# Performance work log

Hardware: AMD Instinct MI355X
Metric: run time of the kernel (lower is better)

The kernel has to match this reference:

```python
import jax, jax.numpy as jnp
import numpy as np

N = 20000
E = 320000
D_IN = 256
D = 128
H = 4
L = 2
NUM_CLASSES = 7
LN_EPS = 1e-5


def setup_inputs() -> dict:
    key = jax.random.key(0)
    ks = jax.random.split(key, 12)
    inp = {}
    inp["x"] = jax.random.normal(ks[0], (N, D_IN), dtype=jnp.float32)
    inp["edge_index"] = jax.random.randint(ks[1], (2, E), 0, N, dtype=jnp.int32)
    inp["W_in"] = jax.random.normal(ks[2], (D_IN, D), dtype=jnp.float32) / np.sqrt(D_IN)
    inp["b_in"] = jnp.zeros((D,), jnp.float32)
    inp["Wq"] = jax.random.normal(ks[3], (L, D, H * D), dtype=jnp.float32) / np.sqrt(D)
    inp["bq"] = jnp.zeros((L, H * D), jnp.float32)
    inp["Wk"] = jax.random.normal(ks[4], (L, D, H * D), dtype=jnp.float32) / np.sqrt(D)
    inp["bk"] = jnp.zeros((L, H * D), jnp.float32)
    inp["Wv"] = jax.random.normal(ks[5], (L, D, H * D), dtype=jnp.float32) / np.sqrt(D)
    inp["bv"] = jnp.zeros((L, H * D), jnp.float32)
    inp["Wskip"] = jax.random.normal(ks[6], (L, D, D), dtype=jnp.float32) / np.sqrt(D)
    inp["bskip"] = jnp.zeros((L, D), jnp.float32)
    inp["ln_g"] = jnp.ones((L, D), jnp.float32)
    inp["ln_b"] = jnp.zeros((L, D), jnp.float32)
    inp["Wc"] = jax.random.normal(ks[7], (D, NUM_CLASSES), dtype=jnp.float32) / np.sqrt(D)
    inp["bc"] = jnp.zeros((NUM_CLASSES,), jnp.float32)
    return inp


def degree_pe(edge_index):
    # degree of source nodes (edge_index[0]), then sinusoidal encoding of the degree
    deg = jax.ops.segment_sum(jnp.ones((E,), jnp.float32), edge_index[0], num_segments=N)
    i = jnp.arange(D, dtype=jnp.float32)
    freq = deg[:, None] / jnp.power(10000.0, i / D)[None, :]  # [N, D]
    return jnp.where((jnp.arange(D) % 2 == 0)[None, :], jnp.sin(freq), jnp.cos(freq))


def transformer_conv(xf, edge_index, Wq, bq, Wk, bk, Wv, bv, Wskip, bskip):
    # PyG TransformerConv: heads=H, concat=False (mean over heads), root_weight=True
    src, dst = edge_index[0], edge_index[1]
    q = (xf @ Wq + bq).reshape(N, H, D)
    k = (xf @ Wk + bk).reshape(N, H, D)
    v = (xf @ Wv + bv).reshape(N, H, D)
    qe = q[dst]                        # [E, H, D]
    ke = k[src]
    ve = v[src]
    scores = jnp.sum(qe * ke, axis=-1) / np.sqrt(D)  # [E, H]
    m = jax.ops.segment_max(scores, dst, num_segments=N)        # [N, H]
    p = jnp.exp(scores - m[dst])
    s = jax.ops.segment_sum(p, dst, num_segments=N)              # [N, H]
    alpha = p / (s[dst] + 1e-16)
    agg = jax.ops.segment_sum(alpha[:, :, None] * ve, dst, num_segments=N)  # [N, H, D]
    out = jnp.mean(agg, axis=1)       # concat=False -> average heads
    return out + xf @ Wskip + bskip   # root skip connection


def layer_norm(x, g, b):
    mu = jnp.mean(x, axis=-1, keepdims=True)
    var = jnp.mean(jnp.square(x - mu), axis=-1, keepdims=True)
    return (x - mu) * jax.lax.rsqrt(var + LN_EPS) * g + b


def reference(x, edge_index, W_in, b_in, Wq, bq, Wk, bk, Wv, bv, Wskip, bskip, ln_g, ln_b, Wc, bc):
    h = x @ W_in + b_in
    h = h + degree_pe(edge_index)
    for l in range(L):
        h_new = transformer_conv(h, edge_index, Wq[l], bq[l], Wk[l], bk[l], Wv[l], bv[l], Wskip[l], bskip[l])
        h = layer_norm(h + h_new, ln_g[l], ln_b[l])
        if l < L - 1:
            h = jax.nn.relu(h)
    return h @ Wc + bc  # [N, num_classes]
```

## Files before the change

kernel.cpp:

```cpp
#include <hip/hip_runtime.h>
#include <math.h>

#define NN 20000
#define EE 320000
#define DIN 256
#define DD 128
#define HHEADS 4
#define NCLS 7

typedef __attribute__((ext_vector_type(8))) __bf16 bf16x8;
typedef __attribute__((ext_vector_type(4))) float f32x4;
typedef __attribute__((ext_vector_type(2))) float f32x2;

__device__ __forceinline__ unsigned short f2bf(float f) {
  union { float f; unsigned int u; } c; c.f = f;
  unsigned int r = c.u + 0x7fffu + ((c.u >> 16) & 1u);
  return (unsigned short)(r >> 16);
}
__device__ __forceinline__ __bf16 f2bf16(float f) {
  union { unsigned short u; __bf16 b; } cv; cv.u = f2bf(f); return cv.b;
}
__device__ __forceinline__ unsigned char fp8enc(float v) {
  return (unsigned char)(__builtin_amdgcn_cvt_pk_fp8_f32(v, 0.f, 0, false) & 0xff);
}

__global__ void zero_ints(int* __restrict__ p, int n) {
  int i = blockIdx.x * blockDim.x + threadIdx.x;
  if (i < n) p[i] = 0;
}

__global__ void count_kernel(const int* __restrict__ ei, int* __restrict__ deg_src,
                             int* __restrict__ cnt_dst) {
  int e = blockIdx.x * blockDim.x + threadIdx.x;
  if (e >= EE) return;
  atomicAdd(&deg_src[ei[e]], 1);
  atomicAdd(&cnt_dst[ei[EE + e]], 1);
}

__global__ __launch_bounds__(1024) void scan_kernel(const int* __restrict__ cnt,
                                                    int* __restrict__ row_ptr,
                                                    int* __restrict__ fillp) {
  __shared__ int wsum[16];
  __shared__ int carry_s;
  const int tid = threadIdx.x;
  const int wid = tid >> 6, lane = tid & 63;
  if (tid == 0) carry_s = 0;
  __syncthreads();
  for (int base = 0; base < NN; base += 1024) {
    int i = base + tid;
    int x = (i < NN) ? cnt[i] : 0;
    int v = x;
#pragma unroll
    for (int off = 1; off < 64; off <<= 1) {
      int t = __shfl_up(v, off);
      if (lane >= off) v += t;
    }
    if (lane == 63) wsum[wid] = v;
    __syncthreads();
    int woff = 0;
    for (int w = 0; w < wid; ++w) woff += wsum[w];
    int excl = carry_s + woff + v - x;
    if (i < NN) { row_ptr[i] = excl; fillp[i] = excl; }
    __syncthreads();
    if (tid == 1023) carry_s += woff + v;
    __syncthreads();
  }
  if (tid == 0) row_ptr[NN] = EE;
}

__global__ void scatter_kernel(const int* __restrict__ ei, int* __restrict__ fillp,
                               int* __restrict__ ssrc) {
  int e = blockIdx.x * blockDim.x + threadIdx.x;
  if (e >= EE) return;
  int s = ei[e], d = ei[EE + e];
  int pos = atomicAdd(&fillp[d], 1);
  ssrc[pos] = s;
}

__global__ void pack_weights(const float* __restrict__ W_in, const float* __restrict__ Wq,
                             const float* __restrict__ Wk, const float* __restrict__ Wv,
                             const float* __restrict__ Wsk, const float* __restrict__ Wc,
                             __bf16* __restrict__ WT) {
  int idx = blockIdx.x * blockDim.x + threadIdx.x;
  if (idx >= 460800) return;
  float val;
  if (idx < 32768) {
    int m = idx >> 8, k = idx & 255;
    val = W_in[k * 128 + m];
  } else if (idx < 458752) {
    int t = idx - 32768;
    int l = t / 212992; int t2 = t - l * 212992;
    int r = t2 >> 7, kk = t2 & 127;
    if (r < 512)       val = Wq[l * 65536 + kk * 512 + r];
    else if (r < 1024) val = Wk[l * 65536 + kk * 512 + (r - 512)];
    else if (r < 1536) val = Wv[l * 65536 + kk * 512 + (r - 1024)];
    else               val = Wsk[l * 16384 + kk * 128 + (r - 1536)];
  } else {
    int t = idx - 458752;
    int r = t >> 7, kk = t & 127;
    val = (r < NCLS) ? Wc[kk * NCLS + r] : 0.f;
  }
  WT[idx] = f2bf16(val);
}

__global__ void pack_bias(const float* __restrict__ bq, const float* __restrict__ bk,
                          const float* __restrict__ bv, const float* __restrict__ bsk,
                          const float* __restrict__ bc, float* __restrict__ bcomb,
                          float* __restrict__ bcpad) {
  int idx = blockIdx.x * blockDim.x + threadIdx.x;
  if (idx < 3328) {
    int l = idx / 1664, r = idx % 1664;
    float v;
    if (r < 512)       v = bq[l * 512 + r];
    else if (r < 1024) v = bk[l * 512 + (r - 512)];
    else if (r < 1536) v = bv[l * 512 + (r - 1024)];
    else               v = bsk[l * 128 + (r - 1536)];
    bcomb[idx] = v;
  } else if (idx < 3344) {
    int r = idx - 3328;
    bcpad[r] = (r < NCLS) ? bc[r] : 0.f;
  }
}

__global__ __launch_bounds__(256) void mfma_gemm_in(
    const float* __restrict__ A, const __bf16* __restrict__ BT,
    const float* __restrict__ bias, float* __restrict__ o_f32,
    __bf16* __restrict__ o_bf0, const int* __restrict__ deg) {
  constexpr int K = 256;
  __shared__ __attribute__((aligned(16))) __bf16 As[64][136];
  __shared__ __attribute__((aligned(16))) __bf16 Bs[128][136];
  const int tid = threadIdx.x;
  const int brow = blockIdx.x * 64;
  const int wave = tid >> 6, lane = tid & 63;
  const int wm = wave & 1, wn = wave >> 1;
  const int lm = lane & 15, lk = (lane >> 4) * 8;
  const int srow16 = tid >> 4;
  const int sc8 = (tid & 15) * 8;
  f32x4 acc[2][4] = {};
  for (int k0 = 0; k0 < K; k0 += 128) {
    if (k0) __syncthreads();
#pragma unroll
    for (int t = 0; t < 4; ++t) {
      int row = t * 16 + srow16;
      int arow = brow + row;
      arow = (arow < NN) ? arow : (NN - 1);
      const float* ap = A + (size_t)arow * K + k0 + sc8;
      float4 a0 = *(const float4*)ap, a1 = *(const float4*)(ap + 4);
      uint4 w;
      w.x = (unsigned)f2bf(a0.x) | ((unsigned)f2bf(a0.y) << 16);
      w.y = (unsigned)f2bf(a0.z) | ((unsigned)f2bf(a0.w) << 16);
      w.z = (unsigned)f2bf(a1.x) | ((unsigned)f2bf(a1.y) << 16);
      w.w = (unsigned)f2bf(a1.z) | ((unsigned)f2bf(a1.w) << 16);
      *reinterpret_cast<uint4*>(&As[row][sc8]) = w;
    }
#pragma unroll
    for (int t = 0; t < 8; ++t) {
      int row = t * 16 + srow16;
      *reinterpret_cast<uint4*>(&Bs[row][sc8]) =
          *reinterpret_cast<const uint4*>(BT + (size_t)row * K + k0 + sc8);
    }
    __syncthreads();
#pragma unroll
    for (int ks = 0; ks < 4; ++ks) {
      bf16x8 af[2], bfr[4];
#pragma unroll
      for (int i = 0; i < 2; ++i)
        af[i] = *reinterpret_cast<const bf16x8*>(&As[wm * 32 + i * 16 + lm][ks * 32 + lk]);
#pragma unroll
      for (int j = 0; j < 4; ++j)
        bfr[j] = *reinterpret_cast<const bf16x8*>(&Bs[wn * 64 + j * 16 + lm][ks * 32 + lk]);
#pragma unroll
      for (int i = 0; i < 2; ++i)
#pragma unroll
        for (int j = 0; j < 4; ++j)
          acc[i][j] = __builtin_amdgcn_mfma_f32_16x16x32_bf16(af[i], bfr[j], acc[i][j], 0, 0, 0);
    }
  }
#pragma unroll
  for (int i = 0; i < 2; ++i) {
#pragma unroll
    for (int j = 0; j < 4; ++j) {
      const int col = wn * 64 + j * 16 + lm;
      const float bb = bias[col];
#pragma unroll
      for (int r = 0; r < 4; ++r) {
        const int row = brow + wm * 32 + i * 16 + (lane >> 4) * 4 + r;
        if (row >= NN) continue;
        float val = acc[i][j][r] + bb;
        float dg = (float)deg[row];
        float freq = dg * __expf(-0.07195578415606394f * (float)col);
        val += (col & 1) ? __cosf(freq) : __sinf(freq);
        o_f32[(size_t)row * DD + col] = val;
        o_bf0[(size_t)row * DD + col] = f2bf16(val);
      }
    }
  }
}

__global__ __launch_bounds__(512) void mfma_gemm_qkv(
    const __bf16* __restrict__ A, const __bf16* __restrict__ BT,
    const float* __restrict__ bias, const float* __restrict__ resid,
    __bf16* __restrict__ o_q, unsigned char* __restrict__ o_fp8,
    float* __restrict__ o_hs) {
  __shared__ __attribute__((aligned(16))) __bf16 Bs[128][136];
  const int tid = threadIdx.x;
  const int brow = blockIdx.x * 128;
  const int bcol = blockIdx.y * 128;
  const int wave = tid >> 6, lane = tid & 63;
  const int wm = wave & 3, wn = wave >> 2;
  const int lm = lane & 15, lk = (lane >> 4) * 8, l4 = (lane >> 4) * 4;
  const int srow32 = tid >> 4;
  const int sc8 = (tid & 15) * 8;

  uint4 breg[4];
#pragma unroll
  for (int t = 0; t < 4; ++t)
    breg[t] = *reinterpret_cast<const uint4*>(BT + (size_t)(bcol + t * 32 + srow32) * 128 + sc8);

  bf16x8 af[2][4];
#pragma unroll
  for (int i = 0; i < 2; ++i) {
    int row = brow + wm * 32 + i * 16 + lm;
    row = (row < NN) ? row : (NN - 1);
    const __bf16* ap = A + (size_t)row * 128 + lk;
#pragma unroll
    for (int ks = 0; ks < 4; ++ks)
      af[i][ks] = *reinterpret_cast<const bf16x8*>(ap + ks * 32);
  }

#pragma unroll
  for (int t = 0; t < 4; ++t)
    *reinterpret_cast<uint4*>(&Bs[t * 32 + srow32][sc8]) = breg[t];
  __syncthreads();

  f32x4 acc[2][4] = {};
#pragma unroll
  for (int ks = 0; ks < 4; ++ks) {
    bf16x8 bfr[4];
#pragma unroll
    for (int j = 0; j < 4; ++j)
      bfr[j] = *reinterpret_cast<const bf16x8*>(&Bs[wn * 64 + j * 16 + lm][ks * 32 + lk]);
#pragma unroll
    for (int i = 0; i < 2; ++i)
#pragma unroll
      for (int j = 0; j < 4; ++j)
        acc[i][j] = __builtin_amdgcn_mfma_f32_16x16x32_bf16(af[i][ks], bfr[j], acc[i][j], 0, 0, 0);
  }

#pragma unroll
  for (int i = 0; i < 2; ++i) {
#pragma unroll
    for (int j = 0; j < 4; ++j) {
      const int col = bcol + wn * 64 + j * 16 + lm;
      const float bb = bias[col];
#pragma unroll
      for (int r = 0; r < 4; ++r) {
        const int row = brow + wm * 32 + i * 16 + l4 + r;
        if (row >= NN) continue;
        float val = acc[i][j][r] + bb;
        if (col < 512) {
          o_q[(size_t)row * 512 + col] = f2bf16(val);
        } else if (col < 1024) {
          int dim = col - 512;
          o_fp8[(size_t)row * 1024 + (dim >> 3) * 16 + (dim & 7)] = fp8enc(val);
        } else if (col < 1536) {
          int dim = col - 1024;
          o_fp8[(size_t)row * 1024 + (dim >> 3) * 16 + 8 + (dim & 7)] = fp8enc(val);
        } else {
          o_hs[(size_t)row * DD + (col - 1536)] =
              val + resid[(size_t)row * DD + (col - 1536)];
        }
      }
    }
  }
}

__global__ __launch_bounds__(256) void mfma_gemm_cls(
    const __bf16* __restrict__ A, const __bf16* __restrict__ BT,
    const float* __restrict__ bias, float* __restrict__ out) {
  __shared__ __attribute__((aligned(16))) __bf16 Bs[16][136];
  const int tid = threadIdx.x;
  const int wave = tid >> 6, lane = tid & 63;
  const int lm = lane & 15, lk = (lane >> 4) * 8, l4 = (lane >> 4) * 4;
  const int brow = blockIdx.x * 128 + wave * 32;
  {
    int srow = tid >> 4, sc8 = (tid & 15) * 8;
    *reinterpret_cast<uint4*>(&Bs[srow][sc8]) =
        *reinterpret_cast<const uint4*>(BT + (size_t)srow * 128 + sc8);
  }
  __syncthreads();
  bf16x8 af[2][4];
#pragma unroll
  for (int i = 0; i < 2; ++i) {
    int row = brow + i * 16 + lm;
    row = (row < NN) ? row : (NN - 1);
    const __bf16* ap = A + (size_t)row * 128 + lk;
#pragma unroll
    for (int ks = 0; ks < 4; ++ks) af[i][ks] = *reinterpret_cast<const bf16x8*>(ap + ks * 32);
  }
  f32x4 acc[2] = {};
#pragma unroll
  for (int ks = 0; ks < 4; ++ks) {
    bf16x8 bfr = *reinterpret_cast<const bf16x8*>(&Bs[lm][ks * 32 + lk]);
#pragma unroll
    for (int i = 0; i < 2; ++i)
      acc[i] = __builtin_amdgcn_mfma_f32_16x16x32_bf16(af[i][ks], bfr, acc[i], 0, 0, 0);
  }
  if (lm < NCLS) {
    const float bb = bias[lm];
#pragma unroll
    for (int i = 0; i < 2; ++i) {
#pragma unroll
      for (int r = 0; r < 4; ++r) {
        int row = brow + i * 16 + l4 + r;
        if (row < NN) out[(size_t)row * NCLS + lm] = acc[i][r] + bb;
      }
    }
  }
}

__device__ __forceinline__ uint4 loadkv(const unsigned char* __restrict__ kv,
                                        const int* __restrict__ ssrc, int ee, int lane) {
  return *reinterpret_cast<const uint4*>(kv + (size_t)ssrc[ee] * 1024 + lane * 16);
}
__device__ __forceinline__ float qdot8(const f32x2 (&qv)[4], unsigned kx, unsigned ky) {
  f32x2 kd0 = __builtin_amdgcn_cvt_pk_f32_fp8((int)kx, false);
  f32x2 kd1 = __builtin_amdgcn_cvt_pk_f32_fp8((int)kx, true);
  f32x2 kd2 = __builtin_amdgcn_cvt_pk_f32_fp8((int)ky, false);
  f32x2 kd3 = __builtin_amdgcn_cvt_pk_f32_fp8((int)ky, true);
  f32x2 d2 = qv[0] * kd0;
  d2 = qv[1] * kd1 + d2;
  d2 = qv[2] * kd2 + d2;
  d2 = qv[3] * kd3 + d2;
  float d = d2[0] + d2[1];
  d += __shfl_xor(d, 1);
  d += __shfl_xor(d, 2);
  d += __shfl_xor(d, 4);
  d += __shfl_xor(d, 8);
  return d;
}
__device__ __forceinline__ void accum8(f32x2 (&a)[4], float& m, float& s, float sc,
                                       unsigned vz, unsigned vw) {
  if (sc > m) {
    float c = __expf(m - sc);
    f32x2 c2 = {c, c};
    s *= c;
#pragma unroll
    for (int d = 0; d < 4; ++d) a[d] *= c2;
    m = sc;
  }
  float w = __expf(sc - m);
  s += w;
  f32x2 w2 = {w, w};
  f32x2 vd0 = __builtin_amdgcn_cvt_pk_f32_fp8((int)vz, false);
  f32x2 vd1 = __builtin_amdgcn_cvt_pk_f32_fp8((int)vz, true);
  f32x2 vd2 = __builtin_amdgcn_cvt_pk_f32_fp8((int)vw, false);
  f32x2 vd3 = __builtin_amdgcn_cvt_pk_f32_fp8((int)vw, true);
  a[0] = w2 * vd0 + a[0];
  a[1] = w2 * vd1 + a[1];
  a[2] = w2 * vd2 + a[2];
  a[3] = w2 * vd3 + a[3];
}

__global__ __launch_bounds__(256) void attn_fused(
    const __bf16* __restrict__ qb, const unsigned char* __restrict__ kv,
    const float* __restrict__ hs,
    const int* __restrict__ row_ptr, const int* __restrict__ ssrc,
    const float* __restrict__ ln_g, const float* __restrict__ ln_b,
    float* __restrict__ h_out, __bf16* __restrict__ hb_out, int relu_flag) {
  const int node = blockIdx.x * 4 + (threadIdx.x >> 6);
  const int lane = threadIdx.x & 63;
  const int grp = lane >> 4, l16 = lane & 15;
  const int e0 = row_ptr[node], e1 = row_ptr[node + 1];
  const float scale = 0.088388347648318447f;

  f32x2 qv[4];
  {
    uint4 qw = *reinterpret_cast<const uint4*>(qb + (size_t)node * 512 + lane * 8);
    union { unsigned u; float f; } c;
    c.u = qw.x << 16; qv[0][0] = c.f; c.u = qw.x & 0xffff0000u; qv[0][1] = c.f;
    c.u = qw.y << 16; qv[1][0] = c.f; c.u = qw.y & 0xffff0000u; qv[1][1] = c.f;
    c.u = qw.z << 16; qv[2][0] = c.f; c.u = qw.z & 0xffff0000u; qv[2][1] = c.f;
    c.u = qw.w << 16; qv[3][0] = c.f; c.u = qw.w & 0xffff0000u; qv[3][1] = c.f;
  }
  float m = -INFINITY, s = 0.f;
  f32x2 a[4] = {};

  uint4 w0, w1, w2, w3;
  if (e0 + 0 < e1) w0 = loadkv(kv, ssrc, e0 + 0, lane);
  if (e0 + 1 < e1) w1 = loadkv(kv, ssrc, e0 + 1, lane);
  if (e0 + 2 < e1) w2 = loadkv(kv, ssrc, e0 + 2, lane);
  if (e0 + 3 < e1) w3 = loadkv(kv, ssrc, e0 + 3, lane);
  int e = e0;
  while (e < e1) {
    {
      float sc = qdot8(qv, w0.x, w0.y) * scale;
      unsigned vz = w0.z, vw = w0.w;
      if (e + 4 < e1) w0 = loadkv(kv, ssrc, e + 4, lane);
      accum8(a, m, s, sc, vz, vw);
    }
    if (e + 1 < e1) {
      float sc = qdot8(qv, w1.x, w1.y) * scale;
      unsigned vz = w1.z, vw = w1.w;
      if (e + 5 < e1) w1 = loadkv(kv, ssrc, e + 5, lane);
      accum8(a, m, s, sc, vz, vw);
    }
    if (e + 2 < e1) {
      float sc = qdot8(qv, w2.x, w2.y) * scale;
      unsigned vz = w2.z, vw = w2.w;
      if (e + 6 < e1) w2 = loadkv(kv, ssrc, e + 6, lane);
      accum8(a, m, s, sc, vz, vw);
    }
    if (e + 3 < e1) {
      float sc = qdot8(qv, w3.x, w3.y) * scale;
      unsigned vz = w3.z, vw = w3.w;
      if (e + 7 < e1) w3 = loadkv(kv, ssrc, e + 7, lane);
      accum8(a, m, s, sc, vz, vw);
    }
    e += 4;
  }

  float inv = 0.25f / (s + 1e-16f);
  float am[8];
#pragma unroll
  for (int d = 0; d < 8; ++d) {
    float ad = a[d >> 1][d & 1] * inv;
    ad += __shfl_xor(ad, 16);
    ad += __shfl_xor(ad, 32);
    am[d] = ad;
  }

  const float4* hp = reinterpret_cast<const float4*>(hs + (size_t)node * DD + l16 * 8);
  float4 h0 = hp[0], h1 = hp[1];
  float val[8];
  val[0] = am[0] + h0.x; val[1] = am[1] + h0.y; val[2] = am[2] + h0.z; val[3] = am[3] + h0.w;
  val[4] = am[4] + h1.x; val[5] = am[5] + h1.y; val[6] = am[6] + h1.z; val[7] = am[7] + h1.w;
  float sum = 0.f, sq = 0.f;
#pragma unroll
  for (int d = 0; d < 8; ++d) { sum += val[d]; sq += val[d] * val[d]; }
  sum += __shfl_xor(sum, 1); sq += __shfl_xor(sq, 1);
  sum += __shfl_xor(sum, 2); sq += __shfl_xor(sq, 2);
  sum += __shfl_xor(sum, 4); sq += __shfl_xor(sq, 4);
  sum += __shfl_xor(sum, 8); sq += __shfl_xor(sq, 8);
  float mu = sum * (1.f / 128.f);
  float var = sq * (1.f / 128.f) - mu * mu;
  float rstd = rsqrtf(var + 1e-5f);

  const float4* gp = reinterpret_cast<const float4*>(ln_g + l16 * 8);
  const float4* bp = reinterpret_cast<const float4*>(ln_b + l16 * 8);
  float4 g0 = gp[0], g1 = gp[1];
  float4 b0 = bp[0], b1 = bp[1];
  float y[8];
  y[0] = (val[0] - mu) * rstd * g0.x + b0.x;
  y[1] = (val[1] - mu) * rstd * g0.y + b0.y;
  y[2] = (val[2] - mu) * rstd * g0.z + b0.z;
  y[3] = (val[3] - mu) * rstd * g0.w + b0.w;
  y[4] = (val[4] - mu) * rstd * g1.x + b1.x;
  y[5] = (val[5] - mu) * rstd * g1.y + b1.y;
  y[6] = (val[6] - mu) * rstd * g1.z + b1.z;
  y[7] = (val[7] - mu) * rstd * g1.w + b1.w;
  if (relu_flag) {
#pragma unroll
    for (int d = 0; d < 8; ++d) y[d] = fmaxf(y[d], 0.f);
  }
  if (grp == 0) {
    float4* op = reinterpret_cast<float4*>(h_out + (size_t)node * DD + l16 * 8);
    op[0] = make_float4(y[0], y[1], y[2], y[3]);
    op[1] = make_float4(y[4], y[5], y[6], y[7]);
  } else if (grp == 1) {
    uint4 w;
    w.x = (unsigned)f2bf(y[0]) | ((unsigned)f2bf(y[1]) << 16);
    w.y = (unsigned)f2bf(y[2]) | ((unsigned)f2bf(y[3]) << 16);
    w.z = (unsigned)f2bf(y[4]) | ((unsigned)f2bf(y[5]) << 16);
    w.w = (unsigned)f2bf(y[6]) | ((unsigned)f2bf(y[7]) << 16);
    *reinterpret_cast<uint4*>(hb_out + (size_t)node * DD + l16 * 8) = w;
  }
}

extern "C" void kernel_launch(void* const* d_in, const int* in_sizes, int n_in,
                              void* d_out, int out_size, void* d_ws, size_t ws_size,
                              hipStream_t stream) {
  const float* x    = (const float*)d_in[0];
  const int*   ei   = (const int*)d_in[1];
  const float* W_in = (const float*)d_in[2];
  const float* b_in = (const float*)d_in[3];
  const float* Wq   = (const float*)d_in[4];
  const float* bq   = (const float*)d_in[5];
  const float* Wk   = (const float*)d_in[6];
  const float* bk   = (const float*)d_in[7];
  const float* Wv   = (const float*)d_in[8];
  const float* bv   = (const float*)d_in[9];
  const float* Wsk  = (const float*)d_in[10];
  const float* bsk  = (const float*)d_in[11];
  const float* ln_g = (const float*)d_in[12];
  const float* ln_b = (const float*)d_in[13];
  const float* Wc   = (const float*)d_in[14];
  const float* bc   = (const float*)d_in[15];
  float* out = (float*)d_out;

  char* ws = (char*)d_ws;
  size_t off = 0;
  float*  hA    = (float*)(ws + off);  off += (size_t)NN * DD * 4;
  float*  hB    = (float*)(ws + off);  off += (size_t)NN * DD * 4;
  __bf16* qb    = (__bf16*)(ws + off); off += (size_t)NN * 512 * 2;
  unsigned char* kvb = (unsigned char*)(ws + off); off += (size_t)NN * 1024;
  float*  hsb   = (float*)(ws + off);  off += (size_t)NN * DD * 4;
  __bf16* hb0   = (__bf16*)(ws + off); off += (size_t)NN * DD * 2;
  __bf16* hb1   = (__bf16*)(ws + off); off += (size_t)NN * DD * 2;
  __bf16* WT    = (__bf16*)(ws + off); off += (size_t)460800 * 2;
  float*  bcomb = (float*)(ws + off);  off += (size_t)3328 * 4;
  float*  bcpad = (float*)(ws + off);  off += (size_t)16 * 4;
  int* deg      = (int*)(ws + off);    off += (size_t)NN * 4;
  int* cnt      = (int*)(ws + off);    off += (size_t)NN * 4;
  int* fillp    = (int*)(ws + off);    off += (size_t)NN * 4;
  int* row_ptr  = (int*)(ws + off);    off += (size_t)(NN + 1) * 4;
  int* ssrc     = (int*)(ws + off);    off += (size_t)EE * 4;

  __bf16* W_inT = WT;
  __bf16* W2T   = WT + 32768;
  __bf16* WcT   = WT + 458752;

  zero_ints<<<(2 * NN + 255) / 256, 256, 0, stream>>>(deg, 2 * NN);
  count_kernel<<<(EE + 255) / 256, 256, 0, stream>>>(ei, deg, cnt);
  scan_kernel<<<1, 1024, 0, stream>>>(cnt, row_ptr, fillp);
  scatter_kernel<<<(EE + 255) / 256, 256, 0, stream>>>(ei, fillp, ssrc);

  pack_weights<<<(460800 + 255) / 256, 256, 0, stream>>>(W_in, Wq, Wk, Wv, Wsk, Wc, WT);
  pack_bias<<<(3344 + 255) / 256, 256, 0, stream>>>(bq, bk, bv, bsk, bc, bcomb, bcpad);

  mfma_gemm_in<<<dim3((NN + 63) / 64, 1), 256, 0, stream>>>(x, W_inT, b_in, hA, hb0, deg);

  const float*  h_in_l[2]   = {hA, hB};
  float*        h_out_l[2]  = {hB, hA};
  const __bf16* hb_in_l[2]  = {hb0, hb1};
  __bf16*       hb_out_l[2] = {hb1, hb0};

  for (int l = 0; l < 2; ++l) {
    dim3 gqkv((NN + 127) / 128, 13);
    mfma_gemm_qkv<<<gqkv, 512, 0, stream>>>(hb_in_l[l], W2T + (size_t)l * 212992,
                                            bcomb + (size_t)l * 1664, h_in_l[l],
                                            qb, kvb, hsb);
    attn_fused<<<NN / 4, 256, 0, stream>>>(qb, kvb, hsb, row_ptr, ssrc,
                                           ln_g + (size_t)l * DD, ln_b + (size_t)l * DD,
                                           h_out_l[l], hb_out_l[l], (l == 0) ? 1 : 0);
  }

  mfma_gemm_cls<<<dim3((NN + 127) / 128, 1), 256, 0, stream>>>(hb0, WcT, bcpad, out);
}
```

Baseline: 318.7 us.

## Stage QKV GEMM epilogue through LDS for coalesced stores and remap blocks per XCD

The QKV GEMM epilogue now writes bf16 Q and fp8 K/V tiles into shared memory first, then stores them to global memory as 16-byte vectors instead of scattered per-element writes. The K/V weight and bias packing is reordered so that each 128-column tile holds interleaved K and V halves matching the fp8 interleaved layout, and the fp8 tile uses an XOR swizzle to reduce bank conflicts. The 2D grid becomes a 1D grid of 2080 blocks whose row index is derived from bid&7, so that blocks sharing the same A rows land on the same XCD for L2 reuse. The cost is extra syncthreads, an LDS round trip, and some blocks that exit early past NN.

```diff
diff --git a/kernel.cpp b/kernel.cpp
--- a/kernel.cpp
+++ b/kernel.cpp
@@ -91,10 +91,17 @@
     int t = idx - 32768;
     int l = t / 212992; int t2 = t - l * 212992;
     int r = t2 >> 7, kk = t2 & 127;
-    if (r < 512)       val = Wq[l * 65536 + kk * 512 + r];
-    else if (r < 1024) val = Wk[l * 65536 + kk * 512 + (r - 512)];
-    else if (r < 1536) val = Wv[l * 65536 + kk * 512 + (r - 1024)];
-    else               val = Wsk[l * 16384 + kk * 128 + (r - 1536)];
+    if (r < 512) {
+      val = Wq[l * 65536 + kk * 512 + r];
+    } else if (r < 1536) {
+      int rr = r - 512;
+      int b = rr >> 7, cc = rr & 127;
+      int dim = b * 64 + (cc & 63);
+      val = (cc >= 64) ? Wv[l * 65536 + kk * 512 + dim]
+                       : Wk[l * 65536 + kk * 512 + dim];
+    } else {
+      val = Wsk[l * 16384 + kk * 128 + (r - 1536)];
+    }
   } else {
     int t = idx - 458752;
     int r = t >> 7, kk = t & 127;
@@ -111,10 +118,16 @@
   if (idx < 3328) {
     int l = idx / 1664, r = idx % 1664;
     float v;
-    if (r < 512)       v = bq[l * 512 + r];
-    else if (r < 1024) v = bk[l * 512 + (r - 512)];
-    else if (r < 1536) v = bv[l * 512 + (r - 1024)];
-    else               v = bsk[l * 128 + (r - 1536)];
+    if (r < 512) {
+      v = bq[l * 512 + r];
+    } else if (r < 1536) {
+      int rr = r - 512;
+      int b = rr >> 7, cc = rr & 127;
+      int dim = b * 64 + (cc & 63);
+      v = (cc >= 64) ? bv[l * 512 + dim] : bk[l * 512 + dim];
+    } else {
+      v = bsk[l * 128 + (r - 1536)];
+    }
     bcomb[idx] = v;
   } else if (idx < 3344) {
     int r = idx - 3328;
@@ -202,10 +215,18 @@
     const float* __restrict__ bias, const float* __restrict__ resid,
     __bf16* __restrict__ o_q, unsigned char* __restrict__ o_fp8,
     float* __restrict__ o_hs) {
-  __shared__ __attribute__((aligned(16))) __bf16 Bs[128][136];
+  __shared__ __attribute__((aligned(16))) unsigned char smem[34816];
+  auto Bs = reinterpret_cast<__bf16(*)[136]>(smem);
+
+  const int bid = blockIdx.x;
+  const int xcd = bid & 7;
+  const int jj = bid >> 3;
+  const int brow128 = xcd * 20 + (jj % 20);
+  if (brow128 * 128 >= NN) return;
+  const int brow = brow128 * 128;
+  const int bcol = (jj / 20) * 128;
+
   const int tid = threadIdx.x;
-  const int brow = blockIdx.x * 128;
-  const int bcol = blockIdx.y * 128;
   const int wave = tid >> 6, lane = tid & 63;
   const int wm = wave & 3, wn = wave >> 2;
   const int lm = lane & 15, lk = (lane >> 4) * 8, l4 = (lane >> 4) * 4;
@@ -247,31 +268,70 @@
         acc[i][j] = __builtin_amdgcn_mfma_f32_16x16x32_bf16(af[i][ks], bfr[j], acc[i][j], 0, 0, 0);
   }
 
-#pragma unroll
-  for (int i = 0; i < 2; ++i) {
-#pragma unroll
-    for (int j = 0; j < 4; ++j) {
-      const int col = bcol + wn * 64 + j * 16 + lm;
-      const float bb = bias[col];
-#pragma unroll
-      for (int r = 0; r < 4; ++r) {
-        const int row = brow + wm * 32 + i * 16 + l4 + r;
-        if (row >= NN) continue;
-        float val = acc[i][j][r] + bb;
-        if (col < 512) {
-          o_q[(size_t)row * 512 + col] = f2bf16(val);
-        } else if (col < 1024) {
-          int dim = col - 512;
-          o_fp8[(size_t)row * 1024 + (dim >> 3) * 16 + (dim & 7)] = fp8enc(val);
-        } else if (col < 1536) {
-          int dim = col - 1024;
-          o_fp8[(size_t)row * 1024 + (dim >> 3) * 16 + 8 + (dim & 7)] = fp8enc(val);
-        } else {
-          o_hs[(size_t)row * DD + (col - 1536)] =
-              val + resid[(size_t)row * DD + (col - 1536)];
+  __syncthreads();
+
+  if (bcol < 512) {
+    auto qt = reinterpret_cast<__bf16(*)[136]>(smem);
+#pragma unroll
+    for (int i = 0; i < 2; ++i)
+#pragma unroll
+      for (int j = 0; j < 4; ++j) {
+        const int cc = wn * 64 + j * 16 + lm;
+        const float bb = bias[bcol + cc];
+#pragma unroll
+        for (int r = 0; r < 4; ++r)
+          qt[wm * 32 + i * 16 + l4 + r][cc] = f2bf16(acc[i][j][r] + bb);
+      }
+    __syncthreads();
+#pragma unroll
+    for (int p = 0; p < 4; ++p) {
+      int slot = tid + p * 512;
+      int row = slot >> 4, c = slot & 15;
+      int grow = brow + row;
+      if (grow < NN)
+        *reinterpret_cast<uint4*>(o_q + (size_t)grow * 512 + bcol + c * 8) =
+            *reinterpret_cast<const uint4*>(&qt[row][c * 8]);
+    }
+  } else if (bcol < 1536) {
+    auto kt = reinterpret_cast<unsigned char(*)[128]>(smem);
+    const int b = (bcol - 512) >> 7;
+#pragma unroll
+    for (int i = 0; i < 2; ++i)
+#pragma unroll
+      for (int j = 0; j < 4; ++j) {
+        const float bb = bias[bcol + wn * 64 + j * 16 + lm];
+        const int boff = (j * 2 + (lm >> 3)) * 16 + wn * 8 + (lm & 7);
+#pragma unroll
+        for (int r = 0; r < 4; ++r) {
+          int lrow = wm * 32 + i * 16 + l4 + r;
+          kt[lrow][boff ^ (((lrow >> 2) & 3) << 5)] = fp8enc(acc[i][j][r] + bb);
         }
       }
-    }
+    __syncthreads();
+#pragma unroll
+    for (int p = 0; p < 2; ++p) {
+      int slot = tid + p * 512;
+      int row = slot >> 3, c = slot & 7;
+      int grow = brow + row;
+      if (grow < NN)
+        *reinterpret_cast<uint4*>(o_fp8 + (size_t)grow * 1024 + b * 128 + c * 16) =
+            *reinterpret_cast<const uint4*>(&kt[row][(c * 16) ^ (((row >> 2) & 3) << 5)]);
+    }
+  } else {
+#pragma unroll
+    for (int i = 0; i < 2; ++i)
+#pragma unroll
+      for (int j = 0; j < 4; ++j) {
+        const int col = bcol + wn * 64 + j * 16 + lm;
+        const float bb = bias[col];
+#pragma unroll
+        for (int r = 0; r < 4; ++r) {
+          const int row = brow + wm * 32 + i * 16 + l4 + r;
+          if (row >= NN) continue;
+          o_hs[(size_t)row * DD + (col - 1536)] =
+              acc[i][j][r] + bb + resid[(size_t)row * DD + (col - 1536)];
+        }
+      }
   }
 }
 
@@ -536,8 +596,7 @@
   __bf16*       hb_out_l[2] = {hb1, hb0};
 
   for (int l = 0; l < 2; ++l) {
-    dim3 gqkv((NN + 127) / 128, 13);
-    mfma_gemm_qkv<<<gqkv, 512, 0, stream>>>(hb_in_l[l], W2T + (size_t)l * 212992,
+    mfma_gemm_qkv<<<2080, 512, 0, stream>>>(hb_in_l[l], W2T + (size_t)l * 212992,
                                             bcomb + (size_t)l * 1664, h_in_l[l],
                                             qb, kvb, hsb);
     attn_fused<<<NN / 4, 256, 0, stream>>>(qb, kvb, hsb, row_ptr, ssrc,
```

After: 290.7 us. -8.8%, faster.
